# Kernel optimization log

Measured on AMD Instinct MI355X. Metric: run time of the kernel, lower is better.

Reference implementation:

```python
import jax, jax.numpy as jnp
import numpy as np
from jax.scipy.linalg import expm

D = 512      # d_model
S = 3        # num_scales
BATCH = 256
H = 8        # attention heads
HD = D // H  # head dim


def layernorm(x, g, b, eps=1e-5):
    m = jnp.mean(x, axis=-1, keepdims=True)
    v = jnp.var(x, axis=-1, keepdims=True)
    return (x - m) / jnp.sqrt(v + eps) * g + b


def setup_inputs() -> dict:
    key = jax.random.key(0)
    ks = jax.random.split(key, 16)
    sd = 1.0 / np.sqrt(D)
    inp = {
        'x': jax.random.normal(ks[0], (BATCH, D), jnp.float32),
        'h_prev': jax.random.normal(ks[1], (BATCH, D), jnp.float32),
        'lstm_h': jax.random.normal(ks[2], (S, BATCH, D), jnp.float32) * 0.1,
        'lstm_c': jax.random.normal(ks[3], (S, BATCH, D), jnp.float32) * 0.1,
        'A': jax.random.normal(ks[4], (D, D), jnp.float32) * sd,
        'Bm': jax.random.normal(ks[5], (D, D), jnp.float32) * sd,
        'dn_w1': jax.random.normal(ks[6], (D, D), jnp.float32) * sd,
        'dn_b1': jnp.zeros((D,), jnp.float32),
        'dn_g': jnp.ones((D,), jnp.float32),
        'dn_beta': jnp.zeros((D,), jnp.float32),
        'dn_w2': jax.random.normal(ks[7], (1, D), jnp.float32) * sd,
        'dn_b2': jnp.zeros((1,), jnp.float32),
        'lstm_wih': jax.random.normal(ks[8], (S, 4 * D, D), jnp.float32) * sd,
        'lstm_whh': jax.random.normal(ks[9], (S, 4 * D, D), jnp.float32) * sd,
        'lstm_bih': jnp.zeros((S, 4 * D), jnp.float32),
        'lstm_bhh': jnp.zeros((S, 4 * D), jnp.float32),
        'decays': jnp.linspace(0.5, 0.95, S, dtype=jnp.float32),
        'attn_in_w': jax.random.normal(ks[10], (3 * D, D), jnp.float32) * sd,
        'attn_in_b': jnp.zeros((3 * D,), jnp.float32),
        'attn_out_w': jax.random.normal(ks[11], (D, D), jnp.float32) * sd,
        'attn_out_b': jnp.zeros((D,), jnp.float32),
        'proj_w': jax.random.normal(ks[12], (D, (S + 2) * D), jnp.float32) * (1.0 / np.sqrt((S + 2) * D)),
        'proj_b': jnp.zeros((D,), jnp.float32),
        'proj_g': jnp.ones((D,), jnp.float32),
        'proj_beta': jnp.zeros((D,), jnp.float32),
    }
    return inp


def reference(x, h_prev, lstm_h, lstm_c, A, Bm, dn_w1, dn_b1, dn_g, dn_beta,
              dn_w2, dn_b2, lstm_wih, lstm_whh, lstm_bih, lstm_bhh, decays,
              attn_in_w, attn_in_b, attn_out_w, attn_out_b,
              proj_w, proj_b, proj_g, proj_beta):
    # ---- delta_net: Linear -> LayerNorm -> GELU(exact) -> Linear -> Softplus ----
    h1 = layernorm(x @ dn_w1.T + dn_b1, dn_g, dn_beta)
    h1 = jax.nn.gelu(h1, approximate=False)
    delta = jax.nn.softplus(h1 @ dn_w2.T + dn_b2)           # (B, 1)

    # ---- SSM update: h_t = expm(delta*A) h_prev + delta*B x ----
    A_disc = jax.vmap(expm)(delta[:, :, None] * A)          # (B, D, D)
    h_ssm = jnp.einsum('bij,bj->bi', A_disc, h_prev) + delta * jnp.einsum('ij,bj->bi', Bm, x)

    # ---- multi-scale LSTM cells (vectorized over scales) ----
    gates = (jnp.einsum('bd,skd->sbk', x, lstm_wih)
             + jnp.einsum('sbd,skd->sbk', lstm_h, lstm_whh)
             + (lstm_bih + lstm_bhh)[:, None, :])           # (S, B, 4D)
    gi, gf, gg, go = jnp.split(gates, 4, axis=-1)
    i_g = jax.nn.sigmoid(gi)
    f_g = jax.nn.sigmoid(gf)
    g_g = jnp.tanh(gg)
    o_g = jax.nn.sigmoid(go)
    c_raw = f_g * lstm_c + i_g * g_g                        # (S, B, D)
    h_new = o_g * jnp.tanh(c_raw)                           # (S, B, D)
    dec = decays[:, None, None]
    c_new = dec * lstm_c + (1.0 - dec) * c_raw              # (S, B, D)

    # ---- fusion attention: 1 query (h_ssm), S keys/values (h_new) ----
    Wq, Wk, Wv = jnp.split(attn_in_w, 3, axis=0)
    bq, bk, bv = jnp.split(attn_in_b, 3, axis=0)
    kv = jnp.transpose(h_new, (1, 0, 2))                    # (B, S, D)
    q = (h_ssm @ Wq.T + bq).reshape(-1, 1, H, HD).transpose(0, 2, 1, 3)   # (B,H,1,HD)
    k = (kv @ Wk.T + bk).reshape(-1, S, H, HD).transpose(0, 2, 1, 3)      # (B,H,S,HD)
    v = (kv @ Wv.T + bv).reshape(-1, S, H, HD).transpose(0, 2, 1, 3)
    scores = jnp.einsum('bhqe,bhke->bhqk', q, k) / np.sqrt(HD)
    attn = jax.nn.softmax(scores, axis=-1)
    ctx = jnp.einsum('bhqk,bhke->bhqe', attn, v)            # (B,H,1,HD)
    ctx = ctx.transpose(0, 2, 1, 3).reshape(-1, D)          # (B, D)
    fused = ctx @ attn_out_w.T + attn_out_b                 # (B, D)

    # ---- output projection over concat [h_ssm, fused, h_1..h_S] ----
    combined = jnp.concatenate([h_ssm, fused] + [h_new[i] for i in range(S)], axis=-1)
    output = layernorm(combined @ proj_w.T + proj_b, proj_g, proj_beta)
    return (output, h_ssm, h_new, c_new)
```

## Files before the change

### kernel.cpp

```cpp
#include <hip/hip_runtime.h>
#include <math.h>

#define DIM 512
#define NB 256
#define KMAX 12

using bf16x8 = __attribute__((ext_vector_type(8))) short;
using f32x4  = __attribute__((ext_vector_type(4))) float;
using float4v = __attribute__((ext_vector_type(4))) float;
using ushort4v = __attribute__((ext_vector_type(4))) unsigned short;

__device__ __forceinline__ unsigned short f2b(float f) {
    union { float f; unsigned int u; } v; v.f = f;
    unsigned int r = v.u + 0x7fffu + ((v.u >> 16) & 1u);
    return (unsigned short)(r >> 16);
}
__device__ __forceinline__ float b2f(unsigned short u) {
    union { unsigned int u; float f; } v; v.u = ((unsigned int)u) << 16;
    return v.f;
}
__device__ __forceinline__ ushort4v f2b4(float4v v) {
    ushort4v o;
    o.x = f2b(v.x); o.y = f2b(v.y); o.z = f2b(v.z); o.w = f2b(v.w);
    return o;
}

__device__ __forceinline__ void block_reduce2(float& s, float& q, float* sb1, float* sb2)
{
    int tid = threadIdx.x;
    #pragma unroll
    for (int off = 32; off > 0; off >>= 1) {
        s += __shfl_down(s, off);
        q += __shfl_down(q, off);
    }
    if ((tid & 63) == 0) { sb1[tid >> 6] = s; sb2[tid >> 6] = q; }
    __syncthreads();
    s = sb1[0] + sb1[1] + sb1[2] + sb1[3];
    q = sb2[0] + sb2[1] + sb2[2] + sb2[3];
    __syncthreads();
}

struct GemmDesc {
    const unsigned short* X;
    const unsigned short* W;
    const float* bias;
    float* Cf;
    unsigned short* Cb;
    unsigned short* Ct;
    int M, N, K, ldX, ldW, ldC, tr_row0, acc;
};
struct GemmArgs { GemmDesc d[6]; };
struct LnParams {
    const float* pre; const float* g; const float* beta;
    const float* w2; const float* b2; float* delta; float* coeff;
    int lnd_y;
};

__global__ __launch_bounds__(256) void gemm_mfma(GemmArgs args, LnParams lp)
{
    __shared__ unsigned short lsA[2][8192];
    __shared__ unsigned short lsB[2][8192];
    __shared__ float sb1[4], sb2[4];

    if ((int)blockIdx.y == lp.lnd_y) {
        int b = blockIdx.x, tid = threadIdx.x;
        int i0 = tid, i1 = tid + 256;
        float x0 = lp.pre[(size_t)b * DIM + i0];
        float x1 = lp.pre[(size_t)b * DIM + i1];
        float s = x0 + x1, q = x0 * x0 + x1 * x1;
        block_reduce2(s, q, sb1, sb2);
        float mean = s * (1.f / DIM);
        float var  = q * (1.f / DIM) - mean * mean;
        float inv  = rsqrtf(var + 1e-5f);
        float y0 = (x0 - mean) * inv * lp.g[i0] + lp.beta[i0];
        float y1 = (x1 - mean) * inv * lp.g[i1] + lp.beta[i1];
        float h0 = 0.5f * y0 * (1.f + erff(y0 * 0.70710678118654752f));
        float h1 = 0.5f * y1 * (1.f + erff(y1 * 0.70710678118654752f));
        float p = h0 * lp.w2[i0] + h1 * lp.w2[i1];
        float dummy = 0.f;
        block_reduce2(p, dummy, sb1, sb2);
        if (tid == 0) {
            float z = p + lp.b2[0];
            float d = (z > 20.f) ? z : log1pf(expf(z));
            lp.delta[b] = d;
            float c = 1.f;
            lp.coeff[b] = 1.f;
            for (int k = 1; k <= KMAX; ++k) { c *= d / (float)k; lp.coeff[k * 256 + b] = c; }
        }
        return;
    }

    GemmDesc de = args.d[blockIdx.y];
    int tn = de.N >> 6;
    int tiles = (de.M >> 6) * tn;
    int t = blockIdx.x;
    if (t >= tiles) return;
    int m0 = (t / tn) << 6;
    int n0 = (t % tn) << 6;

    int tid = threadIdx.x;
    int w = tid >> 6;
    int l = tid & 63;
    int nkt = de.K >> 7;

    int srow = w * 16 + (l >> 2);
    int schk = l & 3;
    const unsigned short* gA = de.X + (size_t)(m0 + srow) * de.ldX + schk * 8;
    const unsigned short* gB = de.W + (size_t)(n0 + srow) * de.ldW + schk * 8;
    unsigned short* lA = &lsA[0][(w * 64 + l) * 8];
    unsigned short* lB = &lsB[0][(w * 64 + l) * 8];

#define STAGE(bufi, kt)                                                          \
    do {                                                                         \
        for (int hh = 0; hh < 4; ++hh) {                                         \
            __builtin_amdgcn_global_load_lds(                                    \
                (const __attribute__((address_space(1))) unsigned int*)(gA + (size_t)(kt) * 128 + hh * 32), \
                (__attribute__((address_space(3))) unsigned int*)(lA + (bufi) * 8192 + hh * 2048), 16, 0, 0); \
            __builtin_amdgcn_global_load_lds(                                    \
                (const __attribute__((address_space(1))) unsigned int*)(gB + (size_t)(kt) * 128 + hh * 32), \
                (__attribute__((address_space(3))) unsigned int*)(lB + (bufi) * 8192 + hh * 2048), 16, 0, 0); \
        }                                                                        \
    } while (0)

    int mbase = (w >> 1) * 32;
    int nbase = (w & 1) * 32;

    f32x4 acc[2][2];
    #pragma unroll
    for (int i = 0; i < 2; ++i)
        #pragma unroll
        for (int j = 0; j < 2; ++j)
            acc[i][j] = (f32x4){0.f, 0.f, 0.f, 0.f};

    int kg = l >> 4;
    int fr = l & 15;
    int aslot = (mbase * 4 + fr * 4 + kg) * 8;
    int bslot = (nbase * 4 + fr * 4 + kg) * 8;

    STAGE(0, 0);

    for (int kt = 0; kt < nkt; ++kt) {
        __syncthreads();
        if (kt + 1 < nkt) STAGE((kt + 1) & 1, kt + 1);

        const unsigned short* bufA = &lsA[kt & 1][0];
        const unsigned short* bufB = &lsB[kt & 1][0];
        #pragma unroll
        for (int h = 0; h < 4; ++h) {
            bf16x8 a0 = *(const bf16x8*)(bufA + h * 2048 + aslot);
            bf16x8 a1 = *(const bf16x8*)(bufA + h * 2048 + aslot + 512);
            bf16x8 b0 = *(const bf16x8*)(bufB + h * 2048 + bslot);
            bf16x8 b1 = *(const bf16x8*)(bufB + h * 2048 + bslot + 512);
            acc[0][0] = __builtin_amdgcn_mfma_f32_16x16x32_bf16(a0, b0, acc[0][0], 0, 0, 0);
            acc[0][1] = __builtin_amdgcn_mfma_f32_16x16x32_bf16(a0, b1, acc[0][1], 0, 0, 0);
            acc[1][0] = __builtin_amdgcn_mfma_f32_16x16x32_bf16(a1, b0, acc[1][0], 0, 0, 0);
            acc[1][1] = __builtin_amdgcn_mfma_f32_16x16x32_bf16(a1, b1, acc[1][1], 0, 0, 0);
        }
    }

    #pragma unroll
    for (int mi = 0; mi < 2; ++mi) {
        #pragma unroll
        for (int ni = 0; ni < 2; ++ni) {
            int col = n0 + nbase + ni * 16 + fr;
            float bv = de.bias ? de.bias[col] : 0.f;
            #pragma unroll
            for (int r = 0; r < 4; ++r) {
                int row = m0 + mbase + mi * 16 + (l >> 4) * 4 + r;
                float v = acc[mi][ni][r] + bv;
                if (de.Cf) {
                    if (de.acc) de.Cf[(size_t)row * de.ldC + col] += v;
                    else        de.Cf[(size_t)row * de.ldC + col] = v;
                } else {
                    de.Cb[(size_t)row * de.ldC + col] = f2b(v);
                }
                if (de.Ct && row >= de.tr_row0)
                    de.Ct[(size_t)col * 512 + (row - de.tr_row0)] = f2b(v);
            }
        }
    }
#undef STAGE
}

#define NSEG 14
struct PrepArgs {
    const float* sA[NSEG]; const float* sB[NSEG]; unsigned short* dst[NSEG];
    int n4[NSEG], dRL4[NSEG], sRLA4[NSEG], sRLB4[NSEG], half4[NSEG], offA[NSEG];
    const float* A; unsigned short* ATb;
};
__global__ __launch_bounds__(256) void prep_kernel(PrepArgs a)
{
    __shared__ float tile[32][33];
    int bid = blockIdx.x, tid = threadIdx.x;
    if (bid < 2048) {
        const int gstride = 2048 * 256;
        int g0 = bid * 256 + tid;
        for (int seg = 0; seg < NSEG; ++seg) {
            int n4 = a.n4[seg];
            const float* sA = a.sA[seg];
            const float* sB = a.sB[seg];
            unsigned short* d = a.dst[seg];
            int dRL4 = a.dRL4[seg], sRLA4 = a.sRLA4[seg], sRLB4 = a.sRLB4[seg];
            int half4 = a.half4[seg], offA = a.offA[seg];
            for (int i = g0; i < n4; i += gstride) {
                int r = i / dRL4, c = i - r * dRL4;
                const float* src = (c < half4)
                    ? sA + ((size_t)r * sRLA4 + offA + c) * 4
                    : sB + ((size_t)r * sRLB4 + (c - half4)) * 4;
                float4v v = *(const float4v*)src;
                *(ushort4v*)(d + (size_t)i * 4) = f2b4(v);
            }
        }
    } else {
        int tt = bid - 2048;
        int bx = tt & 15, by = tt >> 4;
        int tx = tid & 31, ty = tid >> 5;
        #pragma unroll
        for (int i = 0; i < 32; i += 8)
            tile[ty + i][tx] = a.A[(size_t)(by * 32 + ty + i) * 512 + bx * 32 + tx];
        __syncthreads();
        #pragma unroll
        for (int i = 0; i < 32; i += 8)
            a.ATb[(size_t)(bx * 32 + ty + i) * 512 + by * 32 + tx] = f2b(tile[tx][ty + i]);
    }
}

__global__ void pointwise_fused(
    const float* __restrict__ Tm, const float* __restrict__ coeff,
    const float* __restrict__ h_prev, const float* __restrict__ delta,
    const float* __restrict__ Bx, float* __restrict__ hssm,
    unsigned short* __restrict__ combb,
    const float* __restrict__ gates, const float* __restrict__ bih,
    const float* __restrict__ bhh, const float* __restrict__ cin,
    const float* __restrict__ decays,
    float* __restrict__ hout, float* __restrict__ cout)
{
    int idx4 = blockIdx.x * 256 + threadIdx.x;
    int base = idx4 * 4;
    if (base < 131072) {
        int b = base >> 9, i = base & 511;
        const float* Tr = Tm + (size_t)b * (KMAX * DIM) + i;
        float4v a = *(const float4v*)(h_prev + base);
        #pragma unroll
        for (int k = 1; k <= KMAX; ++k) {
            float c = coeff[k * 256 + b];
            float4v t = *(const float4v*)(Tr + (size_t)(k - 1) * DIM);
            a.x += c * t.x; a.y += c * t.y; a.z += c * t.z; a.w += c * t.w;
        }
        float dl = delta[b];
        float4v bx = *(const float4v*)(Bx + base);
        a.x += dl * bx.x; a.y += dl * bx.y; a.z += dl * bx.z; a.w += dl * bx.w;
        *(float4v*)(hssm + base) = a;
        *(ushort4v*)(combb + (size_t)b * 2048 + i) = f2b4(a);
    } else {
        int i2 = base - 131072;
        int s = i2 / (NB * DIM);
        int r = i2 - s * (NB * DIM);
        int b = r >> 9, d = r & 511;
        const float* gr = gates + (size_t)s * 524288 + (size_t)b * 2048 + d;
        const float* bi = bih + s * 2048 + d;
        const float* bh = bhh + s * 2048 + d;
        float4v gi = *(const float4v*)(gr);
        float4v gf = *(const float4v*)(gr + 512);
        float4v gg = *(const float4v*)(gr + 1024);
        float4v go = *(const float4v*)(gr + 1536);
        float4v bi0 = *(const float4v*)(bi),        bh0 = *(const float4v*)(bh);
        float4v bi1 = *(const float4v*)(bi + 512),  bh1 = *(const float4v*)(bh + 512);
        float4v bi2 = *(const float4v*)(bi + 1024), bh2 = *(const float4v*)(bh + 1024);
        float4v bi3 = *(const float4v*)(bi + 1536), bh3 = *(const float4v*)(bh + 1536);
        float4v c = *(const float4v*)(cin + i2);
        float dec = decays[s];
        float4v hn, cn;
        #pragma unroll
        for (int j = 0; j < 4; ++j) {
            float vgi = ((const float*)&gi)[j] + ((const float*)&bi0)[j] + ((const float*)&bh0)[j];
            float vgf = ((const float*)&gf)[j] + ((const float*)&bi1)[j] + ((const float*)&bh1)[j];
            float vgg = ((const float*)&gg)[j] + ((const float*)&bi2)[j] + ((const float*)&bh2)[j];
            float vgo = ((const float*)&go)[j] + ((const float*)&bi3)[j] + ((const float*)&bh3)[j];
            float ig = 1.f / (1.f + expf(-vgi));
            float fg = 1.f / (1.f + expf(-vgf));
            float g_ = tanhf(vgg);
            float og = 1.f / (1.f + expf(-vgo));
            float cc = ((const float*)&c)[j];
            float craw = fg * cc + ig * g_;
            ((float*)&hn)[j] = og * tanhf(craw);
            ((float*)&cn)[j] = dec * cc + (1.f - dec) * craw;
        }
        *(float4v*)(hout + i2) = hn;
        *(float4v*)(cout + i2) = cn;
        *(ushort4v*)(combb + (size_t)b * 2048 + 512 + s * 512 + d) = f2b4(hn);
    }
}

__global__ __launch_bounds__(256) void tail_kernel(
    const unsigned short* __restrict__ qb, const unsigned short* __restrict__ kvb,
    const unsigned short* __restrict__ aout_wb, const float* __restrict__ aout_b,
    const unsigned short* __restrict__ P2b, const float* __restrict__ projA,
    const float* __restrict__ fin_g, const float* __restrict__ fin_beta,
    float* __restrict__ outp)
{
    __shared__ float ctxs[512];
    __shared__ float fusedl[512];
    __shared__ float totals[512];
    __shared__ float sb1[4], sb2[4];
    int b = blockIdx.x, tid = threadIdx.x;

    if (tid < 128) {
        int h = tid >> 4, sub = (tid & 15) * 4;
        int col = h * 64 + sub;
        ushort4v q4 = *(const ushort4v*)(qb + (size_t)b * 512 + col);
        float qf[4] = { b2f(q4.x), b2f(q4.y), b2f(q4.z), b2f(q4.w) };
        float p[3];
        ushort4v k4[3], v4[3];
        #pragma unroll
        for (int s = 0; s < 3; ++s) {
            k4[s] = *(const ushort4v*)(kvb + (size_t)s * 262144 + (size_t)b * 1024 + col);
            v4[s] = *(const ushort4v*)(kvb + (size_t)s * 262144 + (size_t)b * 1024 + 512 + col);
            p[s] = qf[0] * b2f(k4[s].x) + qf[1] * b2f(k4[s].y)
                 + qf[2] * b2f(k4[s].z) + qf[3] * b2f(k4[s].w);
        }
        #pragma unroll
        for (int off = 1; off < 16; off <<= 1) {
            p[0] += __shfl_xor(p[0], off);
            p[1] += __shfl_xor(p[1], off);
            p[2] += __shfl_xor(p[2], off);
        }
        const float scale = 0.125f;
        float p0 = p[0] * scale, p1 = p[1] * scale, p2 = p[2] * scale;
        float m = fmaxf(p0, fmaxf(p1, p2));
        float w0 = expf(p0 - m), w1 = expf(p1 - m), w2 = expf(p2 - m);
        float invs = 1.f / (w0 + w1 + w2);
        ctxs[col + 0] = (w0 * b2f(v4[0].x) + w1 * b2f(v4[1].x) + w2 * b2f(v4[2].x)) * invs;
        ctxs[col + 1] = (w0 * b2f(v4[0].y) + w1 * b2f(v4[1].y) + w2 * b2f(v4[2].y)) * invs;
        ctxs[col + 2] = (w0 * b2f(v4[0].z) + w1 * b2f(v4[1].z) + w2 * b2f(v4[2].z)) * invs;
        ctxs[col + 3] = (w0 * b2f(v4[0].w) + w1 * b2f(v4[1].w) + w2 * b2f(v4[2].w)) * invs;
    }
    __syncthreads();

    for (int jj = tid; jj < 512; jj += 256) {
        float acc = aout_b[jj];
        const unsigned short* wr = aout_wb + (size_t)jj * 512;
        for (int k = 0; k < 512; k += 8) {
            ushort4v w0 = *(const ushort4v*)(wr + k);
            ushort4v w1 = *(const ushort4v*)(wr + k + 4);
            acc += ctxs[k+0]*b2f(w0.x) + ctxs[k+1]*b2f(w0.y)
                 + ctxs[k+2]*b2f(w0.z) + ctxs[k+3]*b2f(w0.w)
                 + ctxs[k+4]*b2f(w1.x) + ctxs[k+5]*b2f(w1.y)
                 + ctxs[k+6]*b2f(w1.z) + ctxs[k+7]*b2f(w1.w);
        }
        fusedl[jj] = acc;
    }
    __syncthreads();

    for (int ii = tid; ii < 512; ii += 256) {
        float acc = projA[(size_t)b * 512 + ii];
        const unsigned short* pr = P2b + (size_t)ii * 512;
        for (int j = 0; j < 512; j += 8) {
            ushort4v w0 = *(const ushort4v*)(pr + j);
            ushort4v w1 = *(const ushort4v*)(pr + j + 4);
            acc += fusedl[j+0]*b2f(w0.x) + fusedl[j+1]*b2f(w0.y)
                 + fusedl[j+2]*b2f(w0.z) + fusedl[j+3]*b2f(w0.w)
                 + fusedl[j+4]*b2f(w1.x) + fusedl[j+5]*b2f(w1.y)
                 + fusedl[j+6]*b2f(w1.z) + fusedl[j+7]*b2f(w1.w);
        }
        totals[ii] = acc;
    }
    __syncthreads();

    float x0 = totals[tid], x1 = totals[tid + 256];
    float s = x0 + x1, q = x0 * x0 + x1 * x1;
    block_reduce2(s, q, sb1, sb2);
    float mean = s * (1.f / DIM);
    float var  = q * (1.f / DIM) - mean * mean;
    float inv  = rsqrtf(var + 1e-5f);
    outp[(size_t)b * DIM + tid]       = (x0 - mean) * inv * fin_g[tid]       + fin_beta[tid];
    outp[(size_t)b * DIM + tid + 256] = (x1 - mean) * inv * fin_g[tid + 256] + fin_beta[tid + 256];
}

extern "C" void kernel_launch(void* const* d_in, const int* in_sizes, int n_in,
                              void* d_out, int out_size, void* d_ws, size_t ws_size,
                              hipStream_t stream)
{
    const float* x        = (const float*)d_in[0];
    const float* h_prev   = (const float*)d_in[1];
    const float* lstm_h   = (const float*)d_in[2];
    const float* lstm_c   = (const float*)d_in[3];
    const float* A        = (const float*)d_in[4];
    const float* Bm       = (const float*)d_in[5];
    const float* dn_w1    = (const float*)d_in[6];
    const float* dn_b1    = (const float*)d_in[7];
    const float* dn_g     = (const float*)d_in[8];
    const float* dn_beta  = (const float*)d_in[9];
    const float* dn_w2    = (const float*)d_in[10];
    const float* dn_b2    = (const float*)d_in[11];
    const float* wih      = (const float*)d_in[12];
    const float* whh      = (const float*)d_in[13];
    const float* bih      = (const float*)d_in[14];
    const float* bhh      = (const float*)d_in[15];
    const float* decays   = (const float*)d_in[16];
    const float* ain_w    = (const float*)d_in[17];
    const float* ain_b    = (const float*)d_in[18];
    const float* aout_w   = (const float*)d_in[19];
    const float* aout_b   = (const float*)d_in[20];
    const float* proj_w   = (const float*)d_in[21];
    const float* proj_b   = (const float*)d_in[22];
    const float* proj_g   = (const float*)d_in[23];
    const float* proj_bt  = (const float*)d_in[24];

    float* out  = (float*)d_out;
    float* hssm = out + 131072;
    float* hnew = out + 262144;
    float* cnew = out + 655360;

    unsigned short* us = (unsigned short*)d_ws;
    unsigned short* hpb     = us;
    unsigned short* ATb     = us + 131072;
    unsigned short* dn_w1b  = us + 393216;
    unsigned short* Bmb     = us + 655360;
    unsigned short* ain_wb  = us + 917504;
    unsigned short* proj_wb = us + 1703936;
    unsigned short* P2b     = us + 2752512;
    unsigned short* aout_wb = us + 3014656;
    unsigned short* Pw      = us + 3276800;
    unsigned short* Qa      = us + 5373952;
    unsigned short* Qb      = us + 5636096;
    unsigned short* Wcat    = us + 5898240;
    unsigned short* Xcat    = us + 12189696;
    unsigned short* combb   = us + 12976128;
    unsigned short* qb      = us + 13500416;
    unsigned short* kvb     = us + 13631488;
    unsigned short* U8b     = us + 14417920;
    float* fbase  = (float*)(us + 14548992);
    float* pre1   = fbase;
    float* delta  = fbase + 131072;
    float* coeff  = fbase + 131328;
    float* Bx     = fbase + 134656;
    float* Tm     = fbase + 265728;
    float* gates  = fbase + 1838592;
    float* projout = pre1;

    LnParams lpOff; lpOff.pre = nullptr; lpOff.g = nullptr; lpOff.beta = nullptr;
    lpOff.w2 = nullptr; lpOff.b2 = nullptr; lpOff.delta = nullptr; lpOff.coeff = nullptr;
    lpOff.lnd_y = -1;

    PrepArgs pa;
    int sidx = 0;
    auto LIN = [&](const float* s, unsigned short* d, int n4) {
        pa.sA[sidx]=s; pa.sB[sidx]=s; pa.dst[sidx]=d; pa.n4[sidx]=n4;
        pa.dRL4[sidx]=n4; pa.sRLA4[sidx]=0; pa.sRLB4[sidx]=0;
        pa.half4[sidx]=n4; pa.offA[sidx]=0; ++sidx;
    };
    LIN(h_prev, hpb,     32768);
    LIN(A,      Pw,      65536);
    LIN(dn_w1,  dn_w1b,  65536);
    LIN(Bm,     Bmb,     65536);
    LIN(ain_w,  ain_wb,  196608);
    LIN(aout_w, aout_wb, 65536);
    pa.sA[sidx]=proj_w; pa.sB[sidx]=proj_w + 1024; pa.dst[sidx]=proj_wb; pa.n4[sidx]=262144;
    pa.dRL4[sidx]=512; pa.sRLA4[sidx]=640; pa.sRLB4[sidx]=640; pa.half4[sidx]=128; pa.offA[sidx]=0; ++sidx;
    pa.sA[sidx]=proj_w; pa.sB[sidx]=proj_w; pa.dst[sidx]=P2b; pa.n4[sidx]=65536;
    pa.dRL4[sidx]=128; pa.sRLA4[sidx]=640; pa.sRLB4[sidx]=640; pa.half4[sidx]=128; pa.offA[sidx]=128; ++sidx;
    for (int s = 0; s < 3; ++s) {
        pa.sA[sidx]=wih + (size_t)s*1048576; pa.sB[sidx]=whh + (size_t)s*1048576;
        pa.dst[sidx]=Wcat + (size_t)s*2097152; pa.n4[sidx]=524288;
        pa.dRL4[sidx]=256; pa.sRLA4[sidx]=128; pa.sRLB4[sidx]=128; pa.half4[sidx]=128; pa.offA[sidx]=0; ++sidx;
    }
    for (int s = 0; s < 3; ++s) {
        pa.sA[sidx]=x; pa.sB[sidx]=lstm_h + (size_t)s*131072;
        pa.dst[sidx]=Xcat + (size_t)s*262144; pa.n4[sidx]=65536;
        pa.dRL4[sidx]=256; pa.sRLA4[sidx]=128; pa.sRLB4[sidx]=128; pa.half4[sidx]=128; pa.offA[sidx]=0; ++sidx;
    }
    pa.A = A; pa.ATb = ATb;
    prep_kernel<<<2304, 256, 0, stream>>>(pa);

    GemmArgs ga;
    ga.d[0] = { Xcat, dn_w1b, dn_b1, pre1, nullptr, nullptr, 256, 512, 512, 1024, 512, 512, 0, 0 };
    ga.d[1] = { Xcat, Bmb,    nullptr, Bx,  nullptr, nullptr, 256, 512, 512, 1024, 512, 512, 0, 0 };
    ga.d[2] = { Pw, ATb, nullptr, nullptr, Pw + 1*262144, Qa, 512, 512, 512, 512, 512, 512, 0, 0 };
    for (int s = 0; s < 3; ++s)
        ga.d[3 + s] = { Xcat + (size_t)s * 262144, Wcat + (size_t)s * 2097152, nullptr,
                        gates + (size_t)s * 524288, nullptr, nullptr, 256, 2048, 1024, 1024, 1024, 2048, 0, 0 };
    gemm_mfma<<<dim3(128, 6), 256, 0, stream>>>(ga, lpOff);

    LnParams lp1 = { pre1, dn_g, dn_beta, dn_w2, dn_b2, delta, coeff, 1 };
    ga.d[0] = { Pw, Qa, nullptr, nullptr, Pw + 2*262144, Qb, 1024, 512, 512, 512, 512, 512, 512, 0 };
    gemm_mfma<<<dim3(256, 2), 256, 0, stream>>>(ga, lp1);

    ga.d[0] = { Pw, Qb, nullptr, nullptr, Pw + 4*262144, nullptr, 2048, 512, 512, 512, 512, 512, 0, 0 };
    gemm_mfma<<<dim3(256, 1), 256, 0, stream>>>(ga, lpOff);

    ga.d[0] = { hpb, Pw, nullptr, Tm, nullptr, nullptr, 256, 4096, 512, 512, 512, 6144, 0, 0 };
    ga.d[1] = { hpb, Pw + 7*262144, nullptr, nullptr, U8b, nullptr, 256, 512, 512, 512, 512, 512, 0, 0 };
    gemm_mfma<<<dim3(256, 2), 256, 0, stream>>>(ga, lpOff);

    ga.d[0] = { U8b, Pw, nullptr, Tm + 4096, nullptr, nullptr, 256, 2048, 512, 512, 512, 6144, 0, 0 };
    gemm_mfma<<<dim3(128, 1), 256, 0, stream>>>(ga, lpOff);

    pointwise_fused<<<512, 256, 0, stream>>>(Tm, coeff, h_prev, delta, Bx, hssm, combb,
                                             gates, bih, bhh, lstm_c, decays, hnew, cnew);

    ga.d[0] = { combb, ain_wb, ain_b, nullptr, qb, nullptr, 256, 512, 512, 2048, 512, 512, 0, 0 };
    for (int s = 0; s < 3; ++s)
        ga.d[1 + s] = { combb + 512 + (size_t)s * 512, ain_wb + 262144, ain_b + 512,
                        nullptr, kvb + (size_t)s * 262144, nullptr, 256, 1024, 512, 2048, 512, 1024, 0, 0 };
    ga.d[4] = { combb, proj_wb, proj_b, projout, nullptr, nullptr, 256, 512, 2048, 2048, 2048, 512, 0, 0 };
    gemm_mfma<<<dim3(64, 5), 256, 0, stream>>>(ga, lpOff);

    tail_kernel<<<256, 256, 0, stream>>>(qb, kvb, aout_wb, aout_b, P2b, projout,
                                         proj_g, proj_bt, out);
}
```

Baseline: 234.2 us.

## Fuse fp32-to-bf16 conversion into GEMM staging and reschedule the kernel graph

The separate prep kernel that converted weights and activations to bf16 is removed. GEMMs now read fp32 operands directly and convert them while staging into LDS. The LSTM gate GEMMs are split into separate input and hidden parts that accumulate with atomics into pre-zeroed buffers. The projection GEMM is split per segment the same way, and the LSTM pointwise work is folded into a GEMM launch. The matrix-power chain is rescheduled to expose more parallel GEMMs per launch, which cuts conversion traffic and launch count. In exchange, fp32 loads bypass the direct global-to-LDS path, conversion is redone per tile, atomics are added, and an extra barrier is added per k-step.

```diff
diff --git a/kernel.cpp b/kernel.cpp
--- a/kernel.cpp
+++ b/kernel.cpp
@@ -47,16 +47,45 @@
     float* Cf;
     unsigned short* Cb;
     unsigned short* Ct;
-    int M, N, K, ldX, ldW, ldC, tr_row0, acc;
+    int M, N, K, ldX, ldW, ldC, tr_row0, acc, xf32, wf32;
 };
-struct GemmArgs { GemmDesc d[6]; };
+struct GemmArgs { GemmDesc d[10]; };
 struct LnParams {
     const float* pre; const float* g; const float* beta;
     const float* w2; const float* b2; float* delta; float* coeff;
     int lnd_y;
 };
-
-__global__ __launch_bounds__(256) void gemm_mfma(GemmArgs args, LnParams lp)
+struct PwParams {
+    const float* gates; const float* bih; const float* bhh; const float* cin;
+    const float* decays; float* hout; float* cout; unsigned short* combb;
+    int pw_y;
+};
+
+__device__ __forceinline__ void stage_op(const unsigned short* Xp, int ld, int f32flag,
+    int row, int schk, int kt, unsigned short* lptr, int bufi)
+{
+    if (f32flag) {
+        const float* Xf = (const float*)Xp;
+        const float* src = Xf + (size_t)row * ld + kt * 128 + schk * 8;
+        #pragma unroll
+        for (int hh = 0; hh < 4; ++hh) {
+            float4v v0 = *(const float4v*)(src + hh * 32);
+            float4v v1 = *(const float4v*)(src + hh * 32 + 4);
+            unsigned short* d = lptr + bufi * 8192 + hh * 2048;
+            *(ushort4v*)d       = f2b4(v0);
+            *(ushort4v*)(d + 4) = f2b4(v1);
+        }
+    } else {
+        const unsigned short* g = Xp + (size_t)row * ld + schk * 8;
+        #pragma unroll
+        for (int hh = 0; hh < 4; ++hh)
+            __builtin_amdgcn_global_load_lds(
+                (const __attribute__((address_space(1))) unsigned int*)(g + (size_t)kt * 128 + hh * 32),
+                (__attribute__((address_space(3))) unsigned int*)(lptr + bufi * 8192 + hh * 2048), 16, 0, 0);
+    }
+}
+
+__global__ __launch_bounds__(256) void gemm_mfma(GemmArgs args, LnParams lp, PwParams pp)
 {
     __shared__ unsigned short lsA[2][8192];
     __shared__ unsigned short lsB[2][8192];
@@ -64,6 +93,7 @@
 
     if ((int)blockIdx.y == lp.lnd_y) {
         int b = blockIdx.x, tid = threadIdx.x;
+        if (b >= 256) return;
         int i0 = tid, i1 = tid + 256;
         float x0 = lp.pre[(size_t)b * DIM + i0];
         float x1 = lp.pre[(size_t)b * DIM + i1];
@@ -89,177 +119,16 @@
         }
         return;
     }
-
-    GemmDesc de = args.d[blockIdx.y];
-    int tn = de.N >> 6;
-    int tiles = (de.M >> 6) * tn;
-    int t = blockIdx.x;
-    if (t >= tiles) return;
-    int m0 = (t / tn) << 6;
-    int n0 = (t % tn) << 6;
-
-    int tid = threadIdx.x;
-    int w = tid >> 6;
-    int l = tid & 63;
-    int nkt = de.K >> 7;
-
-    int srow = w * 16 + (l >> 2);
-    int schk = l & 3;
-    const unsigned short* gA = de.X + (size_t)(m0 + srow) * de.ldX + schk * 8;
-    const unsigned short* gB = de.W + (size_t)(n0 + srow) * de.ldW + schk * 8;
-    unsigned short* lA = &lsA[0][(w * 64 + l) * 8];
-    unsigned short* lB = &lsB[0][(w * 64 + l) * 8];
-
-#define STAGE(bufi, kt)                                                          \
-    do {                                                                         \
-        for (int hh = 0; hh < 4; ++hh) {                                         \
-            __builtin_amdgcn_global_load_lds(                                    \
-                (const __attribute__((address_space(1))) unsigned int*)(gA + (size_t)(kt) * 128 + hh * 32), \
-                (__attribute__((address_space(3))) unsigned int*)(lA + (bufi) * 8192 + hh * 2048), 16, 0, 0); \
-            __builtin_amdgcn_global_load_lds(                                    \
-                (const __attribute__((address_space(1))) unsigned int*)(gB + (size_t)(kt) * 128 + hh * 32), \
-                (__attribute__((address_space(3))) unsigned int*)(lB + (bufi) * 8192 + hh * 2048), 16, 0, 0); \
-        }                                                                        \
-    } while (0)
-
-    int mbase = (w >> 1) * 32;
-    int nbase = (w & 1) * 32;
-
-    f32x4 acc[2][2];
-    #pragma unroll
-    for (int i = 0; i < 2; ++i)
-        #pragma unroll
-        for (int j = 0; j < 2; ++j)
-            acc[i][j] = (f32x4){0.f, 0.f, 0.f, 0.f};
-
-    int kg = l >> 4;
-    int fr = l & 15;
-    int aslot = (mbase * 4 + fr * 4 + kg) * 8;
-    int bslot = (nbase * 4 + fr * 4 + kg) * 8;
-
-    STAGE(0, 0);
-
-    for (int kt = 0; kt < nkt; ++kt) {
-        __syncthreads();
-        if (kt + 1 < nkt) STAGE((kt + 1) & 1, kt + 1);
-
-        const unsigned short* bufA = &lsA[kt & 1][0];
-        const unsigned short* bufB = &lsB[kt & 1][0];
-        #pragma unroll
-        for (int h = 0; h < 4; ++h) {
-            bf16x8 a0 = *(const bf16x8*)(bufA + h * 2048 + aslot);
-            bf16x8 a1 = *(const bf16x8*)(bufA + h * 2048 + aslot + 512);
-            bf16x8 b0 = *(const bf16x8*)(bufB + h * 2048 + bslot);
-            bf16x8 b1 = *(const bf16x8*)(bufB + h * 2048 + bslot + 512);
-            acc[0][0] = __builtin_amdgcn_mfma_f32_16x16x32_bf16(a0, b0, acc[0][0], 0, 0, 0);
-            acc[0][1] = __builtin_amdgcn_mfma_f32_16x16x32_bf16(a0, b1, acc[0][1], 0, 0, 0);
-            acc[1][0] = __builtin_amdgcn_mfma_f32_16x16x32_bf16(a1, b0, acc[1][0], 0, 0, 0);
-            acc[1][1] = __builtin_amdgcn_mfma_f32_16x16x32_bf16(a1, b1, acc[1][1], 0, 0, 0);
-        }
-    }
-
-    #pragma unroll
-    for (int mi = 0; mi < 2; ++mi) {
-        #pragma unroll
-        for (int ni = 0; ni < 2; ++ni) {
-            int col = n0 + nbase + ni * 16 + fr;
-            float bv = de.bias ? de.bias[col] : 0.f;
-            #pragma unroll
-            for (int r = 0; r < 4; ++r) {
-                int row = m0 + mbase + mi * 16 + (l >> 4) * 4 + r;
-                float v = acc[mi][ni][r] + bv;
-                if (de.Cf) {
-                    if (de.acc) de.Cf[(size_t)row * de.ldC + col] += v;
-                    else        de.Cf[(size_t)row * de.ldC + col] = v;
-                } else {
-                    de.Cb[(size_t)row * de.ldC + col] = f2b(v);
-                }
-                if (de.Ct && row >= de.tr_row0)
-                    de.Ct[(size_t)col * 512 + (row - de.tr_row0)] = f2b(v);
-            }
-        }
-    }
-#undef STAGE
-}
-
-#define NSEG 14
-struct PrepArgs {
-    const float* sA[NSEG]; const float* sB[NSEG]; unsigned short* dst[NSEG];
-    int n4[NSEG], dRL4[NSEG], sRLA4[NSEG], sRLB4[NSEG], half4[NSEG], offA[NSEG];
-    const float* A; unsigned short* ATb;
-};
-__global__ __launch_bounds__(256) void prep_kernel(PrepArgs a)
-{
-    __shared__ float tile[32][33];
-    int bid = blockIdx.x, tid = threadIdx.x;
-    if (bid < 2048) {
-        const int gstride = 2048 * 256;
-        int g0 = bid * 256 + tid;
-        for (int seg = 0; seg < NSEG; ++seg) {
-            int n4 = a.n4[seg];
-            const float* sA = a.sA[seg];
-            const float* sB = a.sB[seg];
-            unsigned short* d = a.dst[seg];
-            int dRL4 = a.dRL4[seg], sRLA4 = a.sRLA4[seg], sRLB4 = a.sRLB4[seg];
-            int half4 = a.half4[seg], offA = a.offA[seg];
-            for (int i = g0; i < n4; i += gstride) {
-                int r = i / dRL4, c = i - r * dRL4;
-                const float* src = (c < half4)
-                    ? sA + ((size_t)r * sRLA4 + offA + c) * 4
-                    : sB + ((size_t)r * sRLB4 + (c - half4)) * 4;
-                float4v v = *(const float4v*)src;
-                *(ushort4v*)(d + (size_t)i * 4) = f2b4(v);
-            }
-        }
-    } else {
-        int tt = bid - 2048;
-        int bx = tt & 15, by = tt >> 4;
-        int tx = tid & 31, ty = tid >> 5;
-        #pragma unroll
-        for (int i = 0; i < 32; i += 8)
-            tile[ty + i][tx] = a.A[(size_t)(by * 32 + ty + i) * 512 + bx * 32 + tx];
-        __syncthreads();
-        #pragma unroll
-        for (int i = 0; i < 32; i += 8)
-            a.ATb[(size_t)(bx * 32 + ty + i) * 512 + by * 32 + tx] = f2b(tile[tx][ty + i]);
-    }
-}
-
-__global__ void pointwise_fused(
-    const float* __restrict__ Tm, const float* __restrict__ coeff,
-    const float* __restrict__ h_prev, const float* __restrict__ delta,
-    const float* __restrict__ Bx, float* __restrict__ hssm,
-    unsigned short* __restrict__ combb,
-    const float* __restrict__ gates, const float* __restrict__ bih,
-    const float* __restrict__ bhh, const float* __restrict__ cin,
-    const float* __restrict__ decays,
-    float* __restrict__ hout, float* __restrict__ cout)
-{
-    int idx4 = blockIdx.x * 256 + threadIdx.x;
-    int base = idx4 * 4;
-    if (base < 131072) {
-        int b = base >> 9, i = base & 511;
-        const float* Tr = Tm + (size_t)b * (KMAX * DIM) + i;
-        float4v a = *(const float4v*)(h_prev + base);
-        #pragma unroll
-        for (int k = 1; k <= KMAX; ++k) {
-            float c = coeff[k * 256 + b];
-            float4v t = *(const float4v*)(Tr + (size_t)(k - 1) * DIM);
-            a.x += c * t.x; a.y += c * t.y; a.z += c * t.z; a.w += c * t.w;
-        }
-        float dl = delta[b];
-        float4v bx = *(const float4v*)(Bx + base);
-        a.x += dl * bx.x; a.y += dl * bx.y; a.z += dl * bx.z; a.w += dl * bx.w;
-        *(float4v*)(hssm + base) = a;
-        *(ushort4v*)(combb + (size_t)b * 2048 + i) = f2b4(a);
-    } else {
-        int i2 = base - 131072;
+    if ((int)blockIdx.y == pp.pw_y) {
+        int idx4 = blockIdx.x * 256 + threadIdx.x;
+        if (idx4 >= 98304) return;
+        int i2 = idx4 * 4;
         int s = i2 / (NB * DIM);
         int r = i2 - s * (NB * DIM);
         int b = r >> 9, d = r & 511;
-        const float* gr = gates + (size_t)s * 524288 + (size_t)b * 2048 + d;
-        const float* bi = bih + s * 2048 + d;
-        const float* bh = bhh + s * 2048 + d;
+        const float* gr = pp.gates + (size_t)s * 524288 + (size_t)b * 2048 + d;
+        const float* bi = pp.bih + s * 2048 + d;
+        const float* bh = pp.bhh + s * 2048 + d;
         float4v gi = *(const float4v*)(gr);
         float4v gf = *(const float4v*)(gr + 512);
         float4v gg = *(const float4v*)(gr + 1024);
@@ -268,8 +137,8 @@
         float4v bi1 = *(const float4v*)(bi + 512),  bh1 = *(const float4v*)(bh + 512);
         float4v bi2 = *(const float4v*)(bi + 1024), bh2 = *(const float4v*)(bh + 1024);
         float4v bi3 = *(const float4v*)(bi + 1536), bh3 = *(const float4v*)(bh + 1536);
-        float4v c = *(const float4v*)(cin + i2);
-        float dec = decays[s];
+        float4v c = *(const float4v*)(pp.cin + i2);
+        float dec = pp.decays[s];
         float4v hn, cn;
         #pragma unroll
         for (int j = 0; j < 4; ++j) {
@@ -286,16 +155,152 @@
             ((float*)&hn)[j] = og * tanhf(craw);
             ((float*)&cn)[j] = dec * cc + (1.f - dec) * craw;
         }
-        *(float4v*)(hout + i2) = hn;
-        *(float4v*)(cout + i2) = cn;
-        *(ushort4v*)(combb + (size_t)b * 2048 + 512 + s * 512 + d) = f2b4(hn);
-    }
+        *(float4v*)(pp.hout + i2) = hn;
+        *(float4v*)(pp.cout + i2) = cn;
+        *(ushort4v*)(pp.combb + (size_t)b * 2048 + 512 + s * 512 + d) = f2b4(hn);
+        return;
+    }
+
+    GemmDesc de = args.d[blockIdx.y];
+    int tn = de.N >> 6;
+    int tiles = (de.M >> 6) * tn;
+    int t = blockIdx.x;
+    if (t >= tiles) return;
+    int m0 = (t / tn) << 6;
+    int n0 = (t % tn) << 6;
+
+    int tid = threadIdx.x;
+    int w = tid >> 6;
+    int l = tid & 63;
+    int nkt = de.K >> 7;
+
+    int srow = w * 16 + (l >> 2);
+    int schk = l & 3;
+    unsigned short* lA = &lsA[0][(w * 64 + l) * 8];
+    unsigned short* lB = &lsB[0][(w * 64 + l) * 8];
+
+    int mbase = (w >> 1) * 32;
+    int nbase = (w & 1) * 32;
+
+    f32x4 acc[2][2];
+    #pragma unroll
+    for (int i = 0; i < 2; ++i)
+        #pragma unroll
+        for (int j = 0; j < 2; ++j)
+            acc[i][j] = (f32x4){0.f, 0.f, 0.f, 0.f};
+
+    int kg = l >> 4;
+    int fr = l & 15;
+    int aslot = (mbase * 4 + fr * 4 + kg) * 8;
+    int bslot = (nbase * 4 + fr * 4 + kg) * 8;
+
+    stage_op(de.X, de.ldX, de.xf32, m0 + srow, schk, 0, lA, 0);
+    stage_op(de.W, de.ldW, de.wf32, n0 + srow, schk, 0, lB, 0);
+
+    for (int kt = 0; kt < nkt; ++kt) {
+        __syncthreads();
+        if (kt + 1 < nkt) {
+            stage_op(de.X, de.ldX, de.xf32, m0 + srow, schk, kt + 1, lA, (kt + 1) & 1);
+            stage_op(de.W, de.ldW, de.wf32, n0 + srow, schk, kt + 1, lB, (kt + 1) & 1);
+        }
+        const unsigned short* bufA = &lsA[kt & 1][0];
+        const unsigned short* bufB = &lsB[kt & 1][0];
+        #pragma unroll
+        for (int h = 0; h < 4; ++h) {
+            bf16x8 a0 = *(const bf16x8*)(bufA + h * 2048 + aslot);
+            bf16x8 a1 = *(const bf16x8*)(bufA + h * 2048 + aslot + 512);
+            bf16x8 b0 = *(const bf16x8*)(bufB + h * 2048 + bslot);
+            bf16x8 b1 = *(const bf16x8*)(bufB + h * 2048 + bslot + 512);
+            acc[0][0] = __builtin_amdgcn_mfma_f32_16x16x32_bf16(a0, b0, acc[0][0], 0, 0, 0);
+            acc[0][1] = __builtin_amdgcn_mfma_f32_16x16x32_bf16(a0, b1, acc[0][1], 0, 0, 0);
+            acc[1][0] = __builtin_amdgcn_mfma_f32_16x16x32_bf16(a1, b0, acc[1][0], 0, 0, 0);
+            acc[1][1] = __builtin_amdgcn_mfma_f32_16x16x32_bf16(a1, b1, acc[1][1], 0, 0, 0);
+        }
+        __syncthreads();
+    }
+
+    #pragma unroll
+    for (int mi = 0; mi < 2; ++mi) {
+        #pragma unroll
+        for (int ni = 0; ni < 2; ++ni) {
+            int col = n0 + nbase + ni * 16 + fr;
+            float bv = de.bias ? de.bias[col] : 0.f;
+            #pragma unroll
+            for (int r = 0; r < 4; ++r) {
+                int row = m0 + mbase + mi * 16 + (l >> 4) * 4 + r;
+                float v = acc[mi][ni][r] + bv;
+                if (de.Cf) {
+                    if (de.acc == 2)      atomicAdd(&de.Cf[(size_t)row * de.ldC + col], v);
+                    else if (de.acc == 1) de.Cf[(size_t)row * de.ldC + col] += v;
+                    else                  de.Cf[(size_t)row * de.ldC + col] = v;
+                } else {
+                    de.Cb[(size_t)row * de.ldC + col] = f2b(v);
+                }
+                if (de.Ct && row >= de.tr_row0)
+                    de.Ct[(size_t)col * 512 + (row - de.tr_row0)] = f2b(v);
+            }
+        }
+    }
+}
+
+__global__ __launch_bounds__(256) void prep0(
+    const float* __restrict__ A, unsigned short* __restrict__ ATb,
+    float* __restrict__ gates, const float* __restrict__ proj_b,
+    float* __restrict__ projout)
+{
+    __shared__ float tile[32][33];
+    int bid = blockIdx.x, tid = threadIdx.x;
+    if (bid < 256) {
+        int bx = bid & 15, by = bid >> 4;
+        int tx = tid & 31, ty = tid >> 5;
+        #pragma unroll
+        for (int i = 0; i < 32; i += 8)
+            tile[ty + i][tx] = A[(size_t)(by * 32 + ty + i) * 512 + bx * 32 + tx];
+        __syncthreads();
+        #pragma unroll
+        for (int i = 0; i < 32; i += 8)
+            ATb[(size_t)(bx * 32 + ty + i) * 512 + by * 32 + tx] = f2b(tile[tx][ty + i]);
+    } else {
+        const int gstride = 128 * 256;
+        int g0 = (bid - 256) * 256 + tid;
+        float4v z = (float4v){0.f, 0.f, 0.f, 0.f};
+        for (int i = g0; i < 393216; i += gstride)
+            ((float4v*)gates)[i] = z;
+        for (int i = g0; i < 32768; i += gstride) {
+            float4v pb = *(const float4v*)(proj_b + (i & 127) * 4);
+            ((float4v*)projout)[i] = pb;
+        }
+    }
+}
+
+__global__ __launch_bounds__(256) void pwh_kernel(
+    const float* __restrict__ Tm, const float* __restrict__ coeff,
+    const float* __restrict__ h_prev, const float* __restrict__ delta,
+    const float* __restrict__ Bx, float* __restrict__ hssm,
+    unsigned short* __restrict__ combb)
+{
+    int idx4 = blockIdx.x * 256 + threadIdx.x;
+    int base = idx4 * 4;
+    int b = base >> 9, i = base & 511;
+    const float* Tr = Tm + (size_t)b * (KMAX * DIM) + i;
+    float4v a = *(const float4v*)(h_prev + base);
+    #pragma unroll
+    for (int k = 1; k <= KMAX; ++k) {
+        float c = coeff[k * 256 + b];
+        float4v t = *(const float4v*)(Tr + (size_t)(k - 1) * DIM);
+        a.x += c * t.x; a.y += c * t.y; a.z += c * t.z; a.w += c * t.w;
+    }
+    float dl = delta[b];
+    float4v bx = *(const float4v*)(Bx + base);
+    a.x += dl * bx.x; a.y += dl * bx.y; a.z += dl * bx.z; a.w += dl * bx.w;
+    *(float4v*)(hssm + base) = a;
+    *(ushort4v*)(combb + (size_t)b * 2048 + i) = f2b4(a);
 }
 
 __global__ __launch_bounds__(256) void tail_kernel(
     const unsigned short* __restrict__ qb, const unsigned short* __restrict__ kvb,
-    const unsigned short* __restrict__ aout_wb, const float* __restrict__ aout_b,
-    const unsigned short* __restrict__ P2b, const float* __restrict__ projA,
+    const float* __restrict__ aout_w, const float* __restrict__ aout_b,
+    const float* __restrict__ proj_w, const float* __restrict__ projA,
     const float* __restrict__ fin_g, const float* __restrict__ fin_beta,
     float* __restrict__ outp)
 {
@@ -339,14 +344,12 @@
 
     for (int jj = tid; jj < 512; jj += 256) {
         float acc = aout_b[jj];
-        const unsigned short* wr = aout_wb + (size_t)jj * 512;
+        const float* wr = aout_w + (size_t)jj * 512;
         for (int k = 0; k < 512; k += 8) {
-            ushort4v w0 = *(const ushort4v*)(wr + k);
-            ushort4v w1 = *(const ushort4v*)(wr + k + 4);
-            acc += ctxs[k+0]*b2f(w0.x) + ctxs[k+1]*b2f(w0.y)
-                 + ctxs[k+2]*b2f(w0.z) + ctxs[k+3]*b2f(w0.w)
-                 + ctxs[k+4]*b2f(w1.x) + ctxs[k+5]*b2f(w1.y)
-                 + ctxs[k+6]*b2f(w1.z) + ctxs[k+7]*b2f(w1.w);
+            float4v w0 = *(const float4v*)(wr + k);
+            float4v w1 = *(const float4v*)(wr + k + 4);
+            acc += ctxs[k+0]*w0.x + ctxs[k+1]*w0.y + ctxs[k+2]*w0.z + ctxs[k+3]*w0.w
+                 + ctxs[k+4]*w1.x + ctxs[k+5]*w1.y + ctxs[k+6]*w1.z + ctxs[k+7]*w1.w;
         }
         fusedl[jj] = acc;
     }
@@ -354,14 +357,12 @@
 
     for (int ii = tid; ii < 512; ii += 256) {
         float acc = projA[(size_t)b * 512 + ii];
-        const unsigned short* pr = P2b + (size_t)ii * 512;
+        const float* pr = proj_w + (size_t)ii * 2560 + 512;
         for (int j = 0; j < 512; j += 8) {
-            ushort4v w0 = *(const ushort4v*)(pr + j);
-            ushort4v w1 = *(const ushort4v*)(pr + j + 4);
-            acc += fusedl[j+0]*b2f(w0.x) + fusedl[j+1]*b2f(w0.y)
-                 + fusedl[j+2]*b2f(w0.z) + fusedl[j+3]*b2f(w0.w)
-                 + fusedl[j+4]*b2f(w1.x) + fusedl[j+5]*b2f(w1.y)
-                 + fusedl[j+6]*b2f(w1.z) + fusedl[j+7]*b2f(w1.w);
+            float4v w0 = *(const float4v*)(pr + j);
+            float4v w1 = *(const float4v*)(pr + j + 4);
+            acc += fusedl[j+0]*w0.x + fusedl[j+1]*w0.y + fusedl[j+2]*w0.z + fusedl[j+3]*w0.w
+                 + fusedl[j+4]*w1.x + fusedl[j+5]*w1.y + fusedl[j+6]*w1.z + fusedl[j+7]*w1.w;
         }
         totals[ii] = acc;
     }
@@ -413,99 +414,85 @@
     float* cnew = out + 655360;
 
     unsigned short* us = (unsigned short*)d_ws;
-    unsigned short* hpb     = us;
-    unsigned short* ATb     = us + 131072;
-    unsigned short* dn_w1b  = us + 393216;
-    unsigned short* Bmb     = us + 655360;
-    unsigned short* ain_wb  = us + 917504;
-    unsigned short* proj_wb = us + 1703936;
-    unsigned short* P2b     = us + 2752512;
-    unsigned short* aout_wb = us + 3014656;
-    unsigned short* Pw      = us + 3276800;
-    unsigned short* Qa      = us + 5373952;
-    unsigned short* Qb      = us + 5636096;
-    unsigned short* Wcat    = us + 5898240;
-    unsigned short* Xcat    = us + 12189696;
-    unsigned short* combb   = us + 12976128;
-    unsigned short* qb      = us + 13500416;
-    unsigned short* kvb     = us + 13631488;
-    unsigned short* U8b     = us + 14417920;
-    float* fbase  = (float*)(us + 14548992);
-    float* pre1   = fbase;
-    float* delta  = fbase + 131072;
-    float* coeff  = fbase + 131328;
-    float* Bx     = fbase + 134656;
-    float* Tm     = fbase + 265728;
-    float* gates  = fbase + 1838592;
-    float* projout = pre1;
-
-    LnParams lpOff; lpOff.pre = nullptr; lpOff.g = nullptr; lpOff.beta = nullptr;
-    lpOff.w2 = nullptr; lpOff.b2 = nullptr; lpOff.delta = nullptr; lpOff.coeff = nullptr;
-    lpOff.lnd_y = -1;
-
-    PrepArgs pa;
-    int sidx = 0;
-    auto LIN = [&](const float* s, unsigned short* d, int n4) {
-        pa.sA[sidx]=s; pa.sB[sidx]=s; pa.dst[sidx]=d; pa.n4[sidx]=n4;
-        pa.dRL4[sidx]=n4; pa.sRLA4[sidx]=0; pa.sRLB4[sidx]=0;
-        pa.half4[sidx]=n4; pa.offA[sidx]=0; ++sidx;
-    };
-    LIN(h_prev, hpb,     32768);
-    LIN(A,      Pw,      65536);
-    LIN(dn_w1,  dn_w1b,  65536);
-    LIN(Bm,     Bmb,     65536);
-    LIN(ain_w,  ain_wb,  196608);
-    LIN(aout_w, aout_wb, 65536);
-    pa.sA[sidx]=proj_w; pa.sB[sidx]=proj_w + 1024; pa.dst[sidx]=proj_wb; pa.n4[sidx]=262144;
-    pa.dRL4[sidx]=512; pa.sRLA4[sidx]=640; pa.sRLB4[sidx]=640; pa.half4[sidx]=128; pa.offA[sidx]=0; ++sidx;
-    pa.sA[sidx]=proj_w; pa.sB[sidx]=proj_w; pa.dst[sidx]=P2b; pa.n4[sidx]=65536;
-    pa.dRL4[sidx]=128; pa.sRLA4[sidx]=640; pa.sRLB4[sidx]=640; pa.half4[sidx]=128; pa.offA[sidx]=128; ++sidx;
+    unsigned short* ATb   = us;
+    unsigned short* P     = us + 262144;
+    unsigned short* Qa    = us + 2097152;
+    unsigned short* Qb    = us + 2359296;
+    unsigned short* combb = us + 2621440;
+    unsigned short* qb    = us + 3145728;
+    unsigned short* kvb   = us + 3276800;
+    unsigned short* U8b   = us + 4063232;
+    float* fbase  = (float*)(us + 4194304);
+    float* pre1    = fbase;
+    float* delta   = fbase + 131072;
+    float* coeff   = fbase + 131328;
+    float* Bx      = fbase + 134656;
+    float* Tm      = fbase + 265728;
+    float* gates   = fbase + 1838592;
+    float* projout = fbase + 3411456;
+
+    LnParams lpOff; lpOff.pre=nullptr; lpOff.g=nullptr; lpOff.beta=nullptr;
+    lpOff.w2=nullptr; lpOff.b2=nullptr; lpOff.delta=nullptr; lpOff.coeff=nullptr; lpOff.lnd_y=-1;
+    PwParams ppOff; ppOff.gates=nullptr; ppOff.bih=nullptr; ppOff.bhh=nullptr; ppOff.cin=nullptr;
+    ppOff.decays=nullptr; ppOff.hout=nullptr; ppOff.cout=nullptr; ppOff.combb=nullptr; ppOff.pw_y=-1;
+
+    #define US(p) ((const unsigned short*)(p))
+
+    prep0<<<384, 256, 0, stream>>>(A, ATb, gates, proj_b, projout);
+
+    GemmArgs ga;
+    GemmDesc z0 = { nullptr,nullptr,nullptr,nullptr,nullptr,nullptr, 0,64,128,0,0,0,0,0,0,0 };
+    for (int i = 0; i < 10; ++i) ga.d[i] = z0;
+
+    ga.d[0] = { US(x), US(dn_w1), dn_b1, pre1, nullptr, nullptr, 256,512,512, 512,512,512, 0,0, 1,1 };
+    ga.d[1] = { US(x), US(Bm),   nullptr, Bx,  nullptr, nullptr, 256,512,512, 512,512,512, 0,0, 1,1 };
+    ga.d[2] = { US(A), ATb,      nullptr, nullptr, P, Qa,        512,512,512, 512,512,512, 0,0, 1,0 };
     for (int s = 0; s < 3; ++s) {
-        pa.sA[sidx]=wih + (size_t)s*1048576; pa.sB[sidx]=whh + (size_t)s*1048576;
-        pa.dst[sidx]=Wcat + (size_t)s*2097152; pa.n4[sidx]=524288;
-        pa.dRL4[sidx]=256; pa.sRLA4[sidx]=128; pa.sRLB4[sidx]=128; pa.half4[sidx]=128; pa.offA[sidx]=0; ++sidx;
-    }
+        ga.d[3+s*2]   = { US(x), US(wih + (size_t)s*1048576), nullptr, gates + (size_t)s*524288,
+                          nullptr, nullptr, 256,2048,512, 512,512,2048, 0,2, 1,1 };
+        ga.d[4+s*2]   = { US(lstm_h + (size_t)s*131072), US(whh + (size_t)s*1048576), nullptr,
+                          gates + (size_t)s*524288, nullptr, nullptr, 256,2048,512, 512,512,2048, 0,2, 1,1 };
+    }
+    gemm_mfma<<<dim3(128, 9), 256, 0, stream>>>(ga, lpOff, ppOff);
+
+    for (int i = 0; i < 10; ++i) ga.d[i] = z0;
+    ga.d[0] = { US(A), Qa, nullptr, nullptr, P + 1*262144, nullptr, 512,512,512, 512,512,512, 0,0, 1,0 };
+    ga.d[1] = { P,     Qa, nullptr, nullptr, P + 2*262144, Qb,      512,512,512, 512,512,512, 0,0, 0,0 };
+    LnParams lp1 = { pre1, dn_g, dn_beta, dn_w2, dn_b2, delta, coeff, 2 };
+    PwParams pp1 = { gates, bih, bhh, lstm_c, decays, hnew, cnew, combb, 3 };
+    gemm_mfma<<<dim3(384, 4), 256, 0, stream>>>(ga, lp1, pp1);
+
+    for (int i = 0; i < 10; ++i) ga.d[i] = z0;
+    ga.d[0] = { US(A), Qb, nullptr, nullptr, P + 3*262144, nullptr, 512,512,512, 512,512,512, 0,0, 1,0 };
+    ga.d[1] = { P,     Qb, nullptr, nullptr, P + 4*262144, nullptr, 1536,512,512, 512,512,512, 0,0, 0,0 };
+    ga.d[2] = { US(h_prev), US(A), nullptr, Tm,       nullptr, nullptr, 256,512,512,  512,512,6144, 0,0, 1,1 };
+    ga.d[3] = { US(h_prev), P,     nullptr, Tm + 512, nullptr, nullptr, 256,1536,512, 512,512,6144, 0,0, 1,0 };
     for (int s = 0; s < 3; ++s) {
-        pa.sA[sidx]=x; pa.sB[sidx]=lstm_h + (size_t)s*131072;
-        pa.dst[sidx]=Xcat + (size_t)s*262144; pa.n4[sidx]=65536;
-        pa.dRL4[sidx]=256; pa.sRLA4[sidx]=128; pa.sRLB4[sidx]=128; pa.half4[sidx]=128; pa.offA[sidx]=0; ++sidx;
-    }
-    pa.A = A; pa.ATb = ATb;
-    prep_kernel<<<2304, 256, 0, stream>>>(pa);
-
-    GemmArgs ga;
-    ga.d[0] = { Xcat, dn_w1b, dn_b1, pre1, nullptr, nullptr, 256, 512, 512, 1024, 512, 512, 0, 0 };
-    ga.d[1] = { Xcat, Bmb,    nullptr, Bx,  nullptr, nullptr, 256, 512, 512, 1024, 512, 512, 0, 0 };
-    ga.d[2] = { Pw, ATb, nullptr, nullptr, Pw + 1*262144, Qa, 512, 512, 512, 512, 512, 512, 0, 0 };
-    for (int s = 0; s < 3; ++s)
-        ga.d[3 + s] = { Xcat + (size_t)s * 262144, Wcat + (size_t)s * 2097152, nullptr,
-                        gates + (size_t)s * 524288, nullptr, nullptr, 256, 2048, 1024, 1024, 1024, 2048, 0, 0 };
-    gemm_mfma<<<dim3(128, 6), 256, 0, stream>>>(ga, lpOff);
-
-    LnParams lp1 = { pre1, dn_g, dn_beta, dn_w2, dn_b2, delta, coeff, 1 };
-    ga.d[0] = { Pw, Qa, nullptr, nullptr, Pw + 2*262144, Qb, 1024, 512, 512, 512, 512, 512, 512, 0 };
-    gemm_mfma<<<dim3(256, 2), 256, 0, stream>>>(ga, lp1);
-
-    ga.d[0] = { Pw, Qb, nullptr, nullptr, Pw + 4*262144, nullptr, 2048, 512, 512, 512, 512, 512, 0, 0 };
-    gemm_mfma<<<dim3(256, 1), 256, 0, stream>>>(ga, lpOff);
-
-    ga.d[0] = { hpb, Pw, nullptr, Tm, nullptr, nullptr, 256, 4096, 512, 512, 512, 6144, 0, 0 };
-    ga.d[1] = { hpb, Pw + 7*262144, nullptr, nullptr, U8b, nullptr, 256, 512, 512, 512, 512, 512, 0, 0 };
-    gemm_mfma<<<dim3(256, 2), 256, 0, stream>>>(ga, lpOff);
-
-    ga.d[0] = { U8b, Pw, nullptr, Tm + 4096, nullptr, nullptr, 256, 2048, 512, 512, 512, 6144, 0, 0 };
-    gemm_mfma<<<dim3(128, 1), 256, 0, stream>>>(ga, lpOff);
-
-    pointwise_fused<<<512, 256, 0, stream>>>(Tm, coeff, h_prev, delta, Bx, hssm, combb,
-                                             gates, bih, bhh, lstm_c, decays, hnew, cnew);
-
-    ga.d[0] = { combb, ain_wb, ain_b, nullptr, qb, nullptr, 256, 512, 512, 2048, 512, 512, 0, 0 };
-    for (int s = 0; s < 3; ++s)
-        ga.d[1 + s] = { combb + 512 + (size_t)s * 512, ain_wb + 262144, ain_b + 512,
-                        nullptr, kvb + (size_t)s * 262144, nullptr, 256, 1024, 512, 2048, 512, 1024, 0, 0 };
-    ga.d[4] = { combb, proj_wb, proj_b, projout, nullptr, nullptr, 256, 512, 2048, 2048, 2048, 512, 0, 0 };
-    gemm_mfma<<<dim3(64, 5), 256, 0, stream>>>(ga, lpOff);
-
-    tail_kernel<<<256, 256, 0, stream>>>(qb, kvb, aout_wb, aout_b, P2b, projout,
+        ga.d[4+s] = { combb + 512 + (size_t)s*512, US(ain_w + 262144), ain_b + 512,
+                      nullptr, kvb + (size_t)s*262144, nullptr, 256,1024,512, 2048,512,1024, 0,0, 0,1 };
+        ga.d[7+s] = { combb + 512 + (size_t)s*512, US(proj_w + 1024 + (size_t)s*512), nullptr,
+                      projout, nullptr, nullptr, 256,512,512, 2048,2560,512, 0,2, 0,1 };
+    }
+    gemm_mfma<<<dim3(192, 10), 256, 0, stream>>>(ga, lpOff, ppOff);
+
+    for (int i = 0; i < 10; ++i) ga.d[i] = z0;
+    ga.d[0] = { US(h_prev), P + 3*262144, nullptr, Tm + 4*512, nullptr, nullptr, 256,2048,512, 512,512,6144, 0,0, 1,0 };
+    ga.d[1] = { US(h_prev), P + 6*262144, nullptr, nullptr, U8b, nullptr, 256,512,512, 512,512,512, 0,0, 1,0 };
+    gemm_mfma<<<dim3(128, 2), 256, 0, stream>>>(ga, lpOff, ppOff);
+
+    for (int i = 0; i < 10; ++i) ga.d[i] = z0;
+    ga.d[0] = { U8b, US(A), nullptr, Tm + 8*512, nullptr, nullptr, 256,512,512,  512,512,6144, 0,0, 0,1 };
+    ga.d[1] = { U8b, P,     nullptr, Tm + 9*512, nullptr, nullptr, 256,1536,512, 512,512,6144, 0,0, 0,0 };
+    gemm_mfma<<<dim3(96, 2), 256, 0, stream>>>(ga, lpOff, ppOff);
+
+    pwh_kernel<<<128, 256, 0, stream>>>(Tm, coeff, h_prev, delta, Bx, hssm, combb);
+
+    for (int i = 0; i < 10; ++i) ga.d[i] = z0;
+    ga.d[0] = { combb, US(ain_w),  ain_b,  nullptr, qb, nullptr, 256,512,512, 2048,512,512, 0,0, 0,1 };
+    ga.d[1] = { combb, US(proj_w), nullptr, projout, nullptr, nullptr, 256,512,512, 2048,2560,512, 0,2, 0,1 };
+    gemm_mfma<<<dim3(32, 2), 256, 0, stream>>>(ga, lpOff, ppOff);
+
+    tail_kernel<<<256, 256, 0, stream>>>(qb, kvb, aout_w, aout_b, proj_w, projout,
                                          proj_g, proj_bt, out);
-}
+    #undef US
+}
```

Measured after the change: 266.8 us. +13.9%, slower.
